# Kernel optimization log

Hardware: AMD Instinct MI355X
Metric: run time of the kernel (lower is better)

The kernel has to match this reference:

```python
import jax, jax.numpy as jnp
import numpy as np

T, HID = 2048, 1536
H, DK, DV = 12, 128, 128
KEY_DIM, VAL_DIM = H * DK, H * DV
CONV_K, GEN_RED = 4, 8
EPS = 1e-5


def setup_inputs() -> dict:
    key = jax.random.key(0)
    ks = jax.random.split(key, 12)
    def rn(k, sh, scale):
        return jax.random.normal(k, sh, dtype=jnp.float32) * scale
    inv = HID ** -0.5
    return {
        "hidden_states": rn(ks[0], (T, HID), 1.0),
        "Wq": rn(ks[1], (HID, KEY_DIM), inv),
        "Wk": rn(ks[2], (HID, KEY_DIM), inv),
        "Wv": rn(ks[3], (HID, VAL_DIM), inv),
        "Wb": rn(ks[4], (HID, H), inv),
        "Wa": rn(ks[5], (HID, H), inv),
        "A_log": jnp.log(jax.random.uniform(ks[6], (H,), minval=1e-3, maxval=16.0)),
        "dt_bias": jnp.ones((H,), jnp.float32),
        "Wg1": rn(ks[7], (HID, HID // GEN_RED), inv),
        "Wg2": rn(ks[8], (HID // GEN_RED, VAL_DIM * CONV_K), (HID // GEN_RED) ** -0.5),
        "Wgate": rn(ks[9], (HID, VAL_DIM), inv),
        "norm_weight": jnp.ones((DV,), jnp.float32),
        "Wo": rn(ks[10], (VAL_DIM, HID), VAL_DIM ** -0.5),
    }


def _dynamic_conv(v, hs, Wg1, Wg2):
    # per-token per-channel causal depthwise conv; kernels generated from hidden_states
    w = jax.nn.silu(hs @ Wg1) @ Wg2                    # (T, VAL_DIM*K)
    w = w.reshape(T, VAL_DIM, CONV_K)                  # (T, D, K)
    vpad = jnp.pad(v, ((CONV_K - 1, 0), (0, 0)))       # causal left pad
    windows = jnp.stack([vpad[i:i + T] for i in range(CONV_K)], axis=1)  # (T, K, D)
    return jax.nn.silu(jnp.einsum('tkd,tdk->td', windows, w))


def _gated_delta_rule(q, k, v, g, beta):
    # q,k: (T,H,DK); v: (T,H,DV); g,beta: (T,H)
    scale = DK ** -0.5
    def step(S, inp):
        q_t, k_t, v_t, g_t, b_t = inp
        S = S * jnp.exp(g_t)[:, None, None]            # decay state
        kv = jnp.einsum('hk,hkv->hv', k_t, S)          # k^T S
        S = S + jnp.einsum('hk,hv->hkv', k_t, (v_t - kv) * b_t[:, None])
        o_t = jnp.einsum('hk,hkv->hv', q_t, S) * scale
        return S, o_t
    S0 = jnp.zeros((H, DK, DV), jnp.float32)
    _, o = jax.lax.scan(step, S0, (q, k, v, g, beta))
    return o                                           # (T, H, DV)


def reference(hidden_states, Wq, Wk, Wv, Wb, Wa, A_log, dt_bias,
              Wg1, Wg2, Wgate, norm_weight, Wo):
    hs = hidden_states
    q = jax.nn.silu(hs @ Wq).reshape(T, H, DK)
    k = jax.nn.silu(hs @ Wk).reshape(T, H, DK)
    v = _dynamic_conv(hs @ Wv, hs, Wg1, Wg2).reshape(T, H, DV)
    beta = jax.nn.sigmoid(hs @ Wb)                           # (T, H)
    g = -jnp.exp(A_log) * jax.nn.softplus(hs @ Wa + dt_bias)  # (T, H) log-decay
    o = _gated_delta_rule(q, k, v, g, beta)                  # (T, H, DV)
    # gated RMSNorm over head_v_dim
    gate = (hs @ Wgate).reshape(T, H, DV)
    o = o * jax.lax.rsqrt(jnp.mean(o * o, axis=-1, keepdims=True) + EPS)
    o = o * norm_weight * (gate * jax.nn.sigmoid(gate))
    return o.reshape(T, VAL_DIM) @ Wo
```

## Files before the change

### kernel.cpp

```cpp
#include <hip/hip_runtime.h>
#include <hip/hip_bf16.h>
#include <math.h>

#define T     2048
#define HID   1536
#define NH    12
#define DK    128
#define DV    128
#define CONVK 4
#define CH    64
#define NC    32

typedef __attribute__((ext_vector_type(8))) short bf16x8;
typedef __attribute__((ext_vector_type(8))) _Float16 fp16x8;
typedef __attribute__((ext_vector_type(4))) float floatx4;

__device__ __forceinline__ float siluf(float x) {
    return x / (1.0f + __expf(-x));
}
__device__ __forceinline__ unsigned short f2bf(float f) {
    union { __hip_bfloat16 b; unsigned short u; } cv;
    cv.b = __float2bfloat16(f);
    return cv.u;
}
__device__ __forceinline__ float bf2f(unsigned short u) {
    union { unsigned int u; float f; } cv;
    cv.u = ((unsigned int)u) << 16;
    return cv.f;
}
__device__ __forceinline__ unsigned short f2h(float f) {
    union { _Float16 h; unsigned short u; } cv;
    cv.h = (_Float16)f;
    return cv.u;
}
__device__ __forceinline__ void gl_lds16(const void* g, void* l) {
    __builtin_amdgcn_global_load_lds(
        (const __attribute__((address_space(1))) void*)g,
        (__attribute__((address_space(3))) void*)l, 16, 0, 0);
}
__device__ __forceinline__ void split8_store(const float* xv,
                                             unsigned short* dh, unsigned short* dl) {
    ushort4 h0, h1, l0, l1;
    h0.x = f2bf(xv[0]); l0.x = f2bf(xv[0] - bf2f(h0.x));
    h0.y = f2bf(xv[1]); l0.y = f2bf(xv[1] - bf2f(h0.y));
    h0.z = f2bf(xv[2]); l0.z = f2bf(xv[2] - bf2f(h0.z));
    h0.w = f2bf(xv[3]); l0.w = f2bf(xv[3] - bf2f(h0.w));
    h1.x = f2bf(xv[4]); l1.x = f2bf(xv[4] - bf2f(h1.x));
    h1.y = f2bf(xv[5]); l1.y = f2bf(xv[5] - bf2f(h1.y));
    h1.z = f2bf(xv[6]); l1.z = f2bf(xv[6] - bf2f(h1.z));
    h1.w = f2bf(xv[7]); l1.w = f2bf(xv[7] - bf2f(h1.w));
    *(ushort4*)dh = h0; *(ushort4*)(dh + 4) = h1;
    *(ushort4*)dl = l0; *(ushort4*)(dl + 4) = l1;
}

__global__ __launch_bounds__(256) void splitcast3_kernel(const float* __restrict__ s,
                                                         unsigned short* __restrict__ hi,
                                                         unsigned short* __restrict__ lo,
                                                         unsigned short* __restrict__ h16,
                                                         int n4) {
    int i = blockIdx.x * 256 + threadIdx.x;
    if (i >= n4) return;
    float4 x = ((const float4*)s)[i];
    ushort4 h, l, f;
    h.x = f2bf(x.x); l.x = f2bf(x.x - bf2f(h.x)); f.x = f2h(x.x);
    h.y = f2bf(x.y); l.y = f2bf(x.y - bf2f(h.y)); f.y = f2h(x.y);
    h.z = f2bf(x.z); l.z = f2bf(x.z - bf2f(h.z)); f.z = f2h(x.z);
    h.w = f2bf(x.w); l.w = f2bf(x.w - bf2f(h.w)); f.w = f2h(x.w);
    ((ushort4*)hi)[i] = h;
    ((ushort4*)lo)[i] = l;
    ((ushort4*)h16)[i] = f;
}

__global__ __launch_bounds__(256) void transsplit_kernel(const float* __restrict__ src,
                                                         unsigned short* __restrict__ hi,
                                                         unsigned short* __restrict__ lo,
                                                         int K, int N) {
    __shared__ float tile[32][33];
    const int k0 = blockIdx.y * 32, n0 = blockIdx.x * 32;
    const int tx = threadIdx.x, ty = threadIdx.y;
#pragma unroll
    for (int r = 0; r < 4; ++r) {
        int kk = k0 + ty + 8 * r, nn = n0 + tx;
        tile[ty + 8 * r][tx] = (nn < N) ? src[(size_t)kk * N + nn] : 0.0f;
    }
    __syncthreads();
#pragma unroll
    for (int r = 0; r < 4; ++r) {
        int nn = n0 + ty + 8 * r, kk = k0 + tx;
        if (nn < N) {
            float x = tile[tx][ty + 8 * r];
            unsigned short h = f2bf(x);
            hi[(size_t)nn * K + kk] = h;
            lo[(size_t)nn * K + kk] = f2bf(x - bf2f(h));
        }
    }
}

__global__ __launch_bounds__(256) void transcasth_kernel(const float* __restrict__ src,
                                                         unsigned short* __restrict__ dst,
                                                         int K, int N) {
    __shared__ float tile[32][33];
    const int k0 = blockIdx.y * 32, n0 = blockIdx.x * 32;
    const int tx = threadIdx.x, ty = threadIdx.y;
#pragma unroll
    for (int r = 0; r < 4; ++r) {
        int kk = k0 + ty + 8 * r, nn = n0 + tx;
        tile[ty + 8 * r][tx] = (nn < N) ? src[(size_t)kk * N + nn] : 0.0f;
    }
    __syncthreads();
#pragma unroll
    for (int r = 0; r < 4; ++r) {
        int nn = n0 + ty + 8 * r, kk = k0 + tx;
        if (nn < N) dst[(size_t)nn * K + kk] = f2h(tile[tx][ty + 8 * r]);
    }
}

template<int EPI, int MODE>
__global__ __launch_bounds__(256)
void mgemm(const unsigned short* __restrict__ Ah, const unsigned short* __restrict__ Al,
           const unsigned short* __restrict__ Bh, const unsigned short* __restrict__ Bl,
           int K, int N, float* __restrict__ C, unsigned short* __restrict__ Cb,
           float* __restrict__ qf, float* __restrict__ vf, float* __restrict__ kf,
           unsigned short* __restrict__ gsilb, unsigned short* __restrict__ w1h16,
           float* __restrict__ bgraw)
{
    constexpr int BN   = MODE ? 64 : 128;
    constexpr int BCH  = BN / 16;
    constexpr int NFR  = MODE ? 2 : 4;
    __shared__ unsigned short AsH[2][4096];
    __shared__ unsigned short BsH[2][BCH * 512];
    __shared__ unsigned short AsL[MODE ? 2 : 1][MODE ? 4096 : 4];
    __shared__ unsigned short BsL[MODE ? 2 : 1][MODE ? BCH * 512 : 4];
    const int tid = threadIdx.x;
    const int wave = tid >> 6, lane = tid & 63;
    const int wr = wave >> 1, wc = wave & 1;
    const int lm = lane & 15, lq = lane >> 4;
    const int rowBase = blockIdx.y * 128, colBase = blockIdx.x * BN;

    floatx4 acc[4][NFR];
#pragma unroll
    for (int i = 0; i < 4; ++i)
#pragma unroll
        for (int j = 0; j < NFR; ++j) acc[i][j] = (floatx4){0.f, 0.f, 0.f, 0.f};

    const int mt0 = wave * 2, mt1 = wave * 2 + 1;
    const size_t aOff0 = (size_t)(rowBase + mt0 * 16 + lm) * K + lq * 8;
    const size_t aOff1 = (size_t)(rowBase + mt1 * 16 + lm) * K + lq * 8;
    const size_t bOff0 = (size_t)(colBase + mt0 * 16 + lm) * K + lq * 8;
    const size_t bOff1 = (size_t)(colBase + mt1 * 16 + lm) * K + lq * 8;
    const size_t bOffW = (size_t)(colBase + wave * 16 + lm) * K + lq * 8;

    auto STAGE = [&](int buf, int k0) {
        gl_lds16(Ah + aOff0 + k0, &AsH[buf][mt0 * 512]);
        gl_lds16(Ah + aOff1 + k0, &AsH[buf][mt1 * 512]);
        if (MODE) {
            gl_lds16(Al + aOff0 + k0, &AsL[buf][mt0 * 512]);
            gl_lds16(Al + aOff1 + k0, &AsL[buf][mt1 * 512]);
            gl_lds16(Bh + bOffW + k0, &BsH[buf][wave * 512]);
            gl_lds16(Bl + bOffW + k0, &BsL[buf][wave * 512]);
        } else {
            gl_lds16(Bh + bOff0 + k0, &BsH[buf][mt0 * 512]);
            gl_lds16(Bh + bOff1 + k0, &BsH[buf][mt1 * 512]);
        }
    };

    const int nIter = K >> 5;
    STAGE(0, 0);
    __syncthreads();
    int cur = 0;
    for (int it = 0; it < nIter; ++it) {
        if (it + 1 < nIter) STAGE(cur ^ 1, (it + 1) << 5);
        if (MODE == 0) {
            fp16x8 a[4], b[4];
#pragma unroll
            for (int i = 0; i < 4; ++i) {
                a[i] = *(const fp16x8*)&AsH[cur][(wr * 4 + i) * 512 + lane * 8];
                b[i] = *(const fp16x8*)&BsH[cur][(wc * 4 + i) * 512 + lane * 8];
            }
#pragma unroll
            for (int mi = 0; mi < 4; ++mi)
#pragma unroll
                for (int ni = 0; ni < 4; ++ni)
                    acc[mi][ni] = __builtin_amdgcn_mfma_f32_16x16x32_f16(
                        a[mi], b[ni], acc[mi][ni], 0, 0, 0);
        } else {
            bf16x8 ah[4], al[4], bh[2], bl[2];
#pragma unroll
            for (int i = 0; i < 4; ++i) {
                ah[i] = *(const bf16x8*)&AsH[cur][(wr * 4 + i) * 512 + lane * 8];
                al[i] = *(const bf16x8*)&AsL[cur][(wr * 4 + i) * 512 + lane * 8];
            }
#pragma unroll
            for (int j = 0; j < 2; ++j) {
                bh[j] = *(const bf16x8*)&BsH[cur][(wc * 2 + j) * 512 + lane * 8];
                bl[j] = *(const bf16x8*)&BsL[cur][(wc * 2 + j) * 512 + lane * 8];
            }
#pragma unroll
            for (int mi = 0; mi < 4; ++mi)
#pragma unroll
                for (int ni = 0; ni < 2; ++ni) {
                    acc[mi][ni] = __builtin_amdgcn_mfma_f32_16x16x32_bf16(
                        ah[mi], bh[ni], acc[mi][ni], 0, 0, 0);
                    acc[mi][ni] = __builtin_amdgcn_mfma_f32_16x16x32_bf16(
                        al[mi], bh[ni], acc[mi][ni], 0, 0, 0);
                    acc[mi][ni] = __builtin_amdgcn_mfma_f32_16x16x32_bf16(
                        ah[mi], bl[ni], acc[mi][ni], 0, 0, 0);
                }
        }
        __syncthreads();
        cur ^= 1;
    }

#pragma unroll
    for (int mi = 0; mi < 4; ++mi)
#pragma unroll
        for (int ni = 0; ni < NFR; ++ni) {
            const int col = colBase + wc * (NFR * 16) + ni * 16 + lm;
#pragma unroll
            for (int r = 0; r < 4; ++r) {
                const int row = rowBase + wr * 64 + mi * 16 + lq * 4 + r;
                const float x = acc[mi][ni][r];
                if (EPI == 0) {
                    C[(size_t)row * N + col] = x;
                } else if (EPI == 3) {
                    Cb[(size_t)row * N + col] = f2bf(x);
                } else if (EPI == 1) {
                    if (col < 1536)       qf[(size_t)row * 1536 + col] = siluf(x);
                    else if (col < 3072)  vf[(size_t)row * 1536 + col - 1536] = x;
                    else if (col < 4608)  gsilb[(size_t)row * 1536 + col - 3072] = f2bf(siluf(x));
                    else if (col < 4800)  w1h16[(size_t)row * 192 + col - 4608] = f2h(siluf(x));
                } else {
                    if (col < 1536)       kf[(size_t)row * 1536 + col] = siluf(x);
                    else if (col < 1560)  bgraw[(size_t)row * 24 + col - 1536] = x;
                }
            }
        }
}

__global__ __launch_bounds__(256) void bg2_kernel(const float* __restrict__ bgraw,
                                                  const float* __restrict__ A_log,
                                                  const float* __restrict__ dt_bias,
                                                  float* __restrict__ beta,
                                                  float* __restrict__ g) {
    int idx = blockIdx.x * 256 + threadIdx.x;
    if (idx >= T * 24) return;
    int t = idx / 24, c = idx % 24;
    float x = bgraw[idx];
    if (c < 12) {
        beta[t * NH + c] = 1.0f / (1.0f + __expf(-x));
    } else {
        int h = c - 12;
        float y = x + dt_bias[h];
        float sp = (y > 20.0f) ? y : log1pf(__expf(y));
        g[t * NH + h] = -__expf(A_log[h]) * sp;
    }
}

__global__ __launch_bounds__(256) void conv_kernel(const float* __restrict__ vpre,
                                                   const unsigned short* __restrict__ w,
                                                   float* __restrict__ v) {
    const int idx = blockIdx.x * 256 + threadIdx.x;
    if (idx >= T * HID) return;
    const int t = idx / HID, d = idx % HID;
    const ushort4 wv = *(const ushort4*)(w + (size_t)t * (HID * CONVK) + d * 4);
    const float w4[4] = { bf2f(wv.x), bf2f(wv.y), bf2f(wv.z), bf2f(wv.w) };
    float acc = 0.0f;
#pragma unroll
    for (int i = 0; i < CONVK; i++) {
        const int ts = t - (CONVK - 1) + i;
        if (ts >= 0) acc += vpre[(size_t)ts * HID + d] * w4[i];
    }
    v[idx] = siluf(acc);
}

__global__ __launch_bounds__(256) void prep_kernel(
    const float* __restrict__ q, const float* __restrict__ k,
    unsigned short* __restrict__ Qth, unsigned short* __restrict__ Qtl,
    unsigned short* __restrict__ Kth, unsigned short* __restrict__ Ktl)
{
    __shared__ float KT[128 * 68];
    const int c = blockIdx.x, h = blockIdx.y;
    const int tid = threadIdx.x;
    const size_t tb = (size_t)(h * NC + c) * 8192;

    {
        const int li = tid >> 2, lq4 = tid & 3;
        const float* src = k + (size_t)(c * CH + li) * HID + h * DK + lq4 * 32;
#pragma unroll
        for (int f = 0; f < 8; ++f) {
            float4 x = *(const float4*)(src + f * 4);
            int d0 = lq4 * 32 + f * 4;
            KT[(d0 + 0) * 68 + li] = x.x; KT[(d0 + 1) * 68 + li] = x.y;
            KT[(d0 + 2) * 68 + li] = x.z; KT[(d0 + 3) * 68 + li] = x.w;
        }
    }

#pragma unroll
    for (int e = 0; e < 4; ++e) {
        int u = e * 256 + tid;
        int ch = u >> 6, l = u & 63;
        int i = (ch >> 2) * 16 + (l & 15);
        int dbase = (ch & 3) * 32 + (l >> 4) * 8;
        const float* src = q + (size_t)(c * CH + i) * HID + h * DK + dbase;
        float4 a = *(const float4*)src, b = *(const float4*)(src + 4);
        float xv[8] = {a.x, a.y, a.z, a.w, b.x, b.y, b.z, b.w};
        split8_store(xv, &Qth[tb + ch * 512 + l * 8], &Qtl[tb + ch * 512 + l * 8]);
    }
    __syncthreads();

#pragma unroll
    for (int e = 0; e < 4; ++e) {
        int u = e * 256 + tid;
        int ch = u >> 6, l = u & 63;
        int dk = (ch >> 1) * 16 + (l & 15);
        int ibase = (ch & 1) * 32 + (l >> 4) * 8;
        float4 a = *(const float4*)&KT[dk * 68 + ibase];
        float4 b = *(const float4*)&KT[dk * 68 + ibase + 4];
        float xv[8] = {a.x, a.y, a.z, a.w, b.x, b.y, b.z, b.w};
        split8_store(xv, &Kth[tb + ch * 512 + l * 8], &Ktl[tb + ch * 512 + l * 8]);
    }
}

__global__ __launch_bounds__(256, 1) void chunkloc_kernel(
    const float* __restrict__ q, const float* __restrict__ k, const float* __restrict__ v,
    const float* __restrict__ g, const float* __restrict__ beta,
    float* __restrict__ X1g,
    unsigned short* __restrict__ X2th, unsigned short* __restrict__ X2tl,
    float* __restrict__ Mg, float* __restrict__ csg)
{
    __shared__ unsigned short KhS[64 * 136], KlS[64 * 136];
    __shared__ unsigned short QhS[64 * 136], QlS[64 * 136];
    __shared__ float KT[128 * 68];
    __shared__ float Vs[64 * 132];
    __shared__ float As[64 * 68];
    __shared__ float cs[64], sb[64], sbb[64];

    const int c = blockIdx.x, h = blockIdx.y;
    const int tid = threadIdx.x;
    const int wave = tid >> 6, lane = tid & 63;
    const int lm = lane & 15, lq = lane >> 4;
    const int li = tid >> 2, lq4 = tid & 3;
    const size_t rowbase = (size_t)(c * CH) * HID + h * DK;

    {
        const float* ksrc = k + rowbase + (size_t)li * HID + lq4 * 32;
        const float* qsrc = q + rowbase + (size_t)li * HID + lq4 * 32;
        const float* vsrc = v + (size_t)(c * CH + li) * HID + h * DV + lq4 * 32;
#pragma unroll
        for (int f = 0; f < 8; ++f) {
            float4 kx = *(const float4*)(ksrc + f * 4);
            float4 qx = *(const float4*)(qsrc + f * 4);
            float4 vx = *(const float4*)(vsrc + f * 4);
            const int d0 = lq4 * 32 + f * 4;
            {
                ushort4 hh, ll;
                hh.x = f2bf(kx.x); ll.x = f2bf(kx.x - bf2f(hh.x));
                hh.y = f2bf(kx.y); ll.y = f2bf(kx.y - bf2f(hh.y));
                hh.z = f2bf(kx.z); ll.z = f2bf(kx.z - bf2f(hh.z));
                hh.w = f2bf(kx.w); ll.w = f2bf(kx.w - bf2f(hh.w));
                *(ushort4*)&KhS[li * 136 + d0] = hh;
                *(ushort4*)&KlS[li * 136 + d0] = ll;
            }
            {
                ushort4 hh, ll;
                hh.x = f2bf(qx.x); ll.x = f2bf(qx.x - bf2f(hh.x));
                hh.y = f2bf(qx.y); ll.y = f2bf(qx.y - bf2f(hh.y));
                hh.z = f2bf(qx.z); ll.z = f2bf(qx.z - bf2f(hh.z));
                hh.w = f2bf(qx.w); ll.w = f2bf(qx.w - bf2f(hh.w));
                *(ushort4*)&QhS[li * 136 + d0] = hh;
                *(ushort4*)&QlS[li * 136 + d0] = ll;
            }
            KT[(d0 + 0) * 68 + li] = kx.x;
            KT[(d0 + 1) * 68 + li] = kx.y;
            KT[(d0 + 2) * 68 + li] = kx.z;
            KT[(d0 + 3) * 68 + li] = kx.w;
            *(float4*)&Vs[li * 132 + d0] = vx;
        }
    }
    if (tid < 64) {
        float gv = g[(c * CH + tid) * NH + h];
        float bv = beta[(c * CH + tid) * NH + h];
        float csv = gv;
#pragma unroll
        for (int off = 1; off < 64; off <<= 1) {
            float n = __shfl_up(csv, off);
            if (tid >= off) csv += n;
        }
        cs[tid] = csv; sb[tid] = bv; sbb[tid] = bv * __expf(csv);
    }
    __syncthreads();

    {
        const int ti = wave;
#pragma unroll
        for (int tj = 0; tj < 4; ++tj) {
            floatx4 acc = (floatx4){0.f, 0.f, 0.f, 0.f};
#pragma unroll
            for (int ks = 0; ks < 4; ++ks) {
                bf16x8 a_h = *(const bf16x8*)&KhS[(ti * 16 + lm) * 136 + ks * 32 + lq * 8];
                bf16x8 a_l = *(const bf16x8*)&KlS[(ti * 16 + lm) * 136 + ks * 32 + lq * 8];
                bf16x8 b_h = *(const bf16x8*)&KhS[(tj * 16 + lm) * 136 + ks * 32 + lq * 8];
                bf16x8 b_l = *(const bf16x8*)&KlS[(tj * 16 + lm) * 136 + ks * 32 + lq * 8];
                acc = __builtin_amdgcn_mfma_f32_16x16x32_bf16(a_h, b_h, acc, 0, 0, 0);
                acc = __builtin_amdgcn_mfma_f32_16x16x32_bf16(a_h, b_l, acc, 0, 0, 0);
                acc = __builtin_amdgcn_mfma_f32_16x16x32_bf16(a_l, b_h, acc, 0, 0, 0);
            }
#pragma unroll
            for (int r = 0; r < 4; ++r) {
                const int i = ti * 16 + lq * 4 + r, j = tj * 16 + lm;
                As[i * 68 + j] = (j < i) ? sb[i] * __expf(cs[i] - cs[j]) * acc[r] : 0.0f;
            }
        }
        const size_t mbase = (size_t)(h * NC + c) * CH * CH;
#pragma unroll
        for (int tj = 0; tj < 4; ++tj) {
            floatx4 acc = (floatx4){0.f, 0.f, 0.f, 0.f};
#pragma unroll
            for (int ks = 0; ks < 4; ++ks) {
                bf16x8 a_h = *(const bf16x8*)&QhS[(ti * 16 + lm) * 136 + ks * 32 + lq * 8];
                bf16x8 a_l = *(const bf16x8*)&QlS[(ti * 16 + lm) * 136 + ks * 32 + lq * 8];
                bf16x8 b_h = *(const bf16x8*)&KhS[(tj * 16 + lm) * 136 + ks * 32 + lq * 8];
                bf16x8 b_l = *(const bf16x8*)&KlS[(tj * 16 + lm) * 136 + ks * 32 + lq * 8];
                acc = __builtin_amdgcn_mfma_f32_16x16x32_bf16(a_h, b_h, acc, 0, 0, 0);
                acc = __builtin_amdgcn_mfma_f32_16x16x32_bf16(a_h, b_l, acc, 0, 0, 0);
                acc = __builtin_amdgcn_mfma_f32_16x16x32_bf16(a_l, b_h, acc, 0, 0, 0);
            }
#pragma unroll
            for (int r = 0; r < 4; ++r) {
                const int i = ti * 16 + lq * 4 + r, j = tj * 16 + lm;
                Mg[mbase + (size_t)i * 64 + j] =
                    (j <= i) ? __expf(cs[i] - cs[j]) * acc[r] : 0.0f;
            }
        }
    }

    float xc[64];
    const int col = tid;
    if (col < 128) {
#pragma unroll
        for (int i = 0; i < 64; ++i) xc[i] = sb[i] * Vs[i * 132 + col];
    } else {
        const int dcol = col - 128;
#pragma unroll
        for (int i4 = 0; i4 < 16; ++i4) {
            float4 kq = *(const float4*)&KT[dcol * 68 + i4 * 4];
            xc[i4 * 4 + 0] = sbb[i4 * 4 + 0] * kq.x;
            xc[i4 * 4 + 1] = sbb[i4 * 4 + 1] * kq.y;
            xc[i4 * 4 + 2] = sbb[i4 * 4 + 2] * kq.z;
            xc[i4 * 4 + 3] = sbb[i4 * 4 + 3] * kq.w;
        }
    }
    __syncthreads();

#pragma unroll
    for (int i = 1; i < 64; ++i) {
        float a = xc[i];
#pragma unroll
        for (int j4 = 0; j4 < (i + 3) / 4; ++j4) {
            float4 a4 = *(const float4*)&As[i * 68 + j4 * 4];
            a -= a4.x * xc[j4 * 4 + 0] + a4.y * xc[j4 * 4 + 1]
               + a4.z * xc[j4 * 4 + 2] + a4.w * xc[j4 * 4 + 3];
        }
        xc[i] = a;
    }

    {
        const size_t xbase = (size_t)(h * NC + c) * CH * 128;
        if (col < 128) {
            for (int i = 0; i < 64; ++i) X1g[xbase + (size_t)i * 128 + col] = xc[i];
        } else {
            for (int i = 0; i < 64; ++i) Vs[i * 132 + (col - 128)] = xc[i];
        }
    }
    if (tid < 64) csg[(size_t)(h * NC + c) * CH + tid] = cs[tid];
    __syncthreads();

    {
        const size_t tb = (size_t)(h * NC + c) * 8192;
#pragma unroll
        for (int e = 0; e < 4; ++e) {
            int u = e * 256 + tid;
            int ch = u >> 6, l = u & 63;
            int i = (ch >> 2) * 16 + (l & 15);
            int dbase = (ch & 3) * 32 + (l >> 4) * 8;
            float4 a = *(const float4*)&Vs[i * 132 + dbase];
            float4 b = *(const float4*)&Vs[i * 132 + dbase + 4];
            float xv[8] = {-a.x, -a.y, -a.z, -a.w, -b.x, -b.y, -b.z, -b.w};
            split8_store(xv, &X2th[tb + ch * 512 + l * 8], &X2tl[tb + ch * 512 + l * 8]);
        }
    }
}

__global__ __launch_bounds__(256, 1) void state_kernel(
    const unsigned short* __restrict__ Qth, const unsigned short* __restrict__ Qtl,
    const unsigned short* __restrict__ Kth, const unsigned short* __restrict__ Ktl,
    const unsigned short* __restrict__ X2th, const unsigned short* __restrict__ X2tl,
    float* __restrict__ X1g ,
    const float* __restrict__ csg, float* __restrict__ o)
{
    __shared__ unsigned short XAh[8192], XAl[8192];
    __shared__ unsigned short QAh[8192], QAl[8192];
    __shared__ unsigned short KAh[8192], KAl[8192];
    __shared__ unsigned short SBh[16 * 136], SBl[16 * 136];
    __shared__ unsigned short UBh[16 * 72],  UBl[16 * 72];
    __shared__ float St[16 * 132];
    __shared__ float scs[64];

    const int h = blockIdx.x, db = blockIdx.y;
    const int tid = threadIdx.x;
    const int wave = tid >> 6, lane = tid & 63;
    const int lm = lane & 15, lq = lane >> 4;

    for (int idx = tid; idx < 16 * 132; idx += 256) St[idx] = 0.0f;
    for (int idx = tid; idx < 16 * 136; idx += 256) { SBh[idx] = 0; SBl[idx] = 0; }
    __syncthreads();

    for (int c = 0; c < NC; ++c) {
        const size_t hc = (size_t)(h * NC + c);
        const size_t xb = hc * CH * 128;
        const size_t tb = hc * 8192 + (size_t)lane * 8;

        if (tid < 64) scs[tid] = csg[hc * CH + tid];
#pragma unroll
        for (int i2 = 0; i2 < 4; ++i2) {
            const int ch = wave * 4 + i2;
            gl_lds16(Qth  + tb + ch * 512, &QAh[ch * 512]);
            gl_lds16(Qtl  + tb + ch * 512, &QAl[ch * 512]);
            gl_lds16(X2th + tb + ch * 512, &XAh[ch * 512]);
            gl_lds16(X2tl + tb + ch * 512, &XAl[ch * 512]);
            gl_lds16(Kth  + tb + ch * 512, &KAh[ch * 512]);
            gl_lds16(Ktl  + tb + ch * 512, &KAl[ch * 512]);
        }
        __syncthreads();

        {
            const int mw = wave;
            float x1r[4];
#pragma unroll
            for (int r = 0; r < 4; ++r)
                x1r[r] = X1g[xb + (size_t)(mw * 16 + lq * 4 + r) * 128 + db * 16 + lm];
            floatx4 accU = (floatx4){0.f, 0.f, 0.f, 0.f};
            floatx4 accO = (floatx4){0.f, 0.f, 0.f, 0.f};
#pragma unroll
            for (int ks = 0; ks < 4; ++ks) {
                bf16x8 xh = *(const bf16x8*)&XAh[(mw * 4 + ks) * 512 + lane * 8];
                bf16x8 xl = *(const bf16x8*)&XAl[(mw * 4 + ks) * 512 + lane * 8];
                bf16x8 qh = *(const bf16x8*)&QAh[(mw * 4 + ks) * 512 + lane * 8];
                bf16x8 ql = *(const bf16x8*)&QAl[(mw * 4 + ks) * 512 + lane * 8];
                bf16x8 sh = *(const bf16x8*)&SBh[lm * 136 + ks * 32 + lq * 8];
                bf16x8 sl = *(const bf16x8*)&SBl[lm * 136 + ks * 32 + lq * 8];
                accU = __builtin_amdgcn_mfma_f32_16x16x32_bf16(xh, sh, accU, 0, 0, 0);
                accU = __builtin_amdgcn_mfma_f32_16x16x32_bf16(xh, sl, accU, 0, 0, 0);
                accU = __builtin_amdgcn_mfma_f32_16x16x32_bf16(xl, sh, accU, 0, 0, 0);
                accO = __builtin_amdgcn_mfma_f32_16x16x32_bf16(qh, sh, accO, 0, 0, 0);
                accO = __builtin_amdgcn_mfma_f32_16x16x32_bf16(qh, sl, accO, 0, 0, 0);
                accO = __builtin_amdgcn_mfma_f32_16x16x32_bf16(ql, sh, accO, 0, 0, 0);
            }
            const float cs63 = scs[63];
#pragma unroll
            for (int r = 0; r < 4; ++r) {
                const int row = mw * 16 + lq * 4 + r;
                const float u = accU[r] + x1r[r];
                X1g[xb + (size_t)row * 128 + db * 16 + lm] = u;
                const float up = u * __expf(cs63 - scs[row]);
                unsigned short uh = f2bf(up);
                UBh[lm * 72 + row] = uh;
                UBl[lm * 72 + row] = f2bf(up - bf2f(uh));
                o[(size_t)(c * CH + row) * HID + h * DV + db * 16 + lm] =
                    __expf(scs[row]) * accO[r];
            }
        }
        __syncthreads();

        {
            const float bC = __expf(scs[63]);
#pragma unroll
            for (int mt2 = 0; mt2 < 2; ++mt2) {
                const int mt = wave * 2 + mt2;
                floatx4 acc;
#pragma unroll
                for (int r = 0; r < 4; ++r)
                    acc[r] = bC * St[lm * 132 + mt * 16 + lq * 4 + r];
#pragma unroll
                for (int ks = 0; ks < 2; ++ks) {
                    bf16x8 ah = *(const bf16x8*)&KAh[(mt * 2 + ks) * 512 + lane * 8];
                    bf16x8 al = *(const bf16x8*)&KAl[(mt * 2 + ks) * 512 + lane * 8];
                    bf16x8 bh = *(const bf16x8*)&UBh[lm * 72 + ks * 32 + lq * 8];
                    bf16x8 bl = *(const bf16x8*)&UBl[lm * 72 + ks * 32 + lq * 8];
                    acc = __builtin_amdgcn_mfma_f32_16x16x32_bf16(ah, bh, acc, 0, 0, 0);
                    acc = __builtin_amdgcn_mfma_f32_16x16x32_bf16(ah, bl, acc, 0, 0, 0);
                    acc = __builtin_amdgcn_mfma_f32_16x16x32_bf16(al, bh, acc, 0, 0, 0);
                }
#pragma unroll
                for (int r = 0; r < 4; ++r) {
                    const int dk = mt * 16 + lq * 4 + r;
                    const float sv = acc[r];
                    St[lm * 132 + dk] = sv;
                    unsigned short sh = f2bf(sv);
                    SBh[lm * 136 + dk] = sh;
                    SBl[lm * 136 + dk] = f2bf(sv - bf2f(sh));
                }
            }
        }
        __syncthreads();
    }
}

__global__ __launch_bounds__(256) void outk_kernel(
    const float* __restrict__ Ug, const float* __restrict__ Mg,
    float* __restrict__ o)
{
    __shared__ float Msh[64 * 68];
    __shared__ float Ush[64 * 68];

    const int c = blockIdx.x, h = blockIdx.y;
    const int dvb = blockIdx.z * 64;
    const int tid = threadIdx.x;
    const size_t hc = (size_t)(h * NC + c);

    for (int e = 0; e < 16; ++e) {
        int idx = e * 256 + tid;
        Msh[(idx >> 6) * 68 + (idx & 63)] = Mg[hc * CH * CH + idx];
    }
    for (int e = 0; e < 16; ++e) {
        int idx = e * 256 + tid;
        int j = idx >> 6, cc = idx & 63;
        Ush[j * 68 + cc] = Ug[hc * CH * 128 + (size_t)j * 128 + dvb + cc];
    }
    __syncthreads();

    const int tx = tid & 15, ty = tid >> 4;
    const int c0 = tx * 4, i0 = ty * 4;
    float acc[4][4] = {{0}};
    for (int j4 = 0; j4 < 16; ++j4) {
        float uv[4][4];
#pragma unroll
        for (int s = 0; s < 4; ++s) {
            float4 u4 = *(const float4*)&Ush[(j4 * 4 + s) * 68 + c0];
            uv[s][0] = u4.x; uv[s][1] = u4.y; uv[s][2] = u4.z; uv[s][3] = u4.w;
        }
#pragma unroll
        for (int r = 0; r < 4; ++r) {
            float4 m4 = *(const float4*)&Msh[(i0 + r) * 68 + j4 * 4];
            const float mv[4] = {m4.x, m4.y, m4.z, m4.w};
#pragma unroll
            for (int s = 0; s < 4; ++s)
#pragma unroll
                for (int e = 0; e < 4; ++e) acc[r][e] += mv[s] * uv[s][e];
        }
    }
    const float scale = 0.08838834764831845f;
#pragma unroll
    for (int r = 0; r < 4; ++r) {
        float* op = &o[(size_t)(c * CH + i0 + r) * HID + h * DV + dvb + c0];
        float4 prev = *(const float4*)op;
        float4 ov = make_float4(scale * (prev.x + acc[r][0]),
                                scale * (prev.y + acc[r][1]),
                                scale * (prev.z + acc[r][2]),
                                scale * (prev.w + acc[r][3]));
        *(float4*)op = ov;
    }
}

__global__ __launch_bounds__(256) void normgate_kernel(const float* __restrict__ o,
                                                       const unsigned short* __restrict__ gsil,
                                                       const float* __restrict__ nw,
                                                       unsigned short* __restrict__ out_hi,
                                                       unsigned short* __restrict__ out_lo) {
    const int gw = (blockIdx.x * 256 + threadIdx.x) >> 6;
    const int lane = threadIdx.x & 63;
    if (gw >= T * NH) return;
    const int t = gw / NH, h = gw % NH;
    const size_t base = (size_t)t * HID + h * DV;
    const float a = o[base + lane];
    const float b = o[base + lane + 64];
    float ss = a * a + b * b;
    ss += __shfl_xor(ss, 1);  ss += __shfl_xor(ss, 2);  ss += __shfl_xor(ss, 4);
    ss += __shfl_xor(ss, 8);  ss += __shfl_xor(ss, 16); ss += __shfl_xor(ss, 32);
    const float r = rsqrtf(ss * (1.0f / 128.0f) + 1e-5f);
    float va = a * r * nw[lane]      * bf2f(gsil[base + lane]);
    float vb = b * r * nw[lane + 64] * bf2f(gsil[base + lane + 64]);
    unsigned short ha = f2bf(va), hb = f2bf(vb);
    out_hi[base + lane]      = ha;  out_lo[base + lane]      = f2bf(va - bf2f(ha));
    out_hi[base + lane + 64] = hb;  out_lo[base + lane + 64] = f2bf(vb - bf2f(hb));
}

extern "C" void kernel_launch(void* const* d_in, const int* in_sizes, int n_in,
                              void* d_out, int out_size, void* d_ws, size_t ws_size,
                              hipStream_t stream) {
    const float* hs      = (const float*)d_in[0];
    const float* Wq      = (const float*)d_in[1];
    const float* Wk      = (const float*)d_in[2];
    const float* Wv      = (const float*)d_in[3];
    const float* Wb      = (const float*)d_in[4];
    const float* Wa      = (const float*)d_in[5];
    const float* A_log   = (const float*)d_in[6];
    const float* dt_bias = (const float*)d_in[7];
    const float* Wg1     = (const float*)d_in[8];
    const float* Wg2     = (const float*)d_in[9];
    const float* Wgate   = (const float*)d_in[10];
    const float* norm_w  = (const float*)d_in[11];
    const float* Wo      = (const float*)d_in[12];

    float* ws = (float*)d_ws;
    float* q    = ws;
    float* kbuf = ws + 3145728;
    float* vpre = ws + 6291456;
    float* vbuf = ws + 9437184;
    unsigned short* gsil = (unsigned short*)(ws + 12582912);
    float* X1g  = ws + 14155776;
    unsigned short* X2th = (unsigned short*)(ws + 17301504);
    unsigned short* X2tl = (unsigned short*)(ws + 18874368);
    float* Mg   = ws + 20447232;
    unsigned short* WTAfh = (unsigned short*)(ws + 14155776);
    unsigned short* WTBh  = (unsigned short*)(ws + 17891328);
    unsigned short* WTBl  = (unsigned short*)(ws + 19169280);
    unsigned short* wcv   = (unsigned short*)(ws + 14155776);
    unsigned short* WG2h  = (unsigned short*)(ws + 22044672);
    unsigned short* hsh   = (unsigned short*)(ws + 22634496);
    unsigned short* w1h16 = (unsigned short*)(ws + 24207360);
    float* bgraw = ws + 24403968;
    unsigned short* Kth = (unsigned short*)(ws + 22044672);
    unsigned short* Ktl = (unsigned short*)(ws + 23617536);
    float* beta  = ws + 25190400;
    float* g     = ws + 25214976;
    float* csg   = ws + 25239552;
    unsigned short* hsbh = (unsigned short*)(ws + 9437184);
    unsigned short* hsbl = (unsigned short*)(ws + 11010048);
    unsigned short* Qth  = (unsigned short*)(ws + 6291456);
    unsigned short* Qtl  = (unsigned short*)(ws + 7864320);
    unsigned short* WoTh = (unsigned short*)(ws);
    unsigned short* WoTl = (unsigned short*)(ws + 1179648);
    unsigned short* onh  = (unsigned short*)(ws + 6291456);
    unsigned short* onl  = (unsigned short*)(ws + 7864320);

    const dim3 blk(256);
    const dim3 blkT(32, 8);

    splitcast3_kernel<<<3072, blk, 0, stream>>>(hs, hsbh, hsbl, hsh, (T * HID) / 4);
    transcasth_kernel<<<dim3(48, 48), blkT, 0, stream>>>(Wq,    WTAfh,               1536, 1536);
    transcasth_kernel<<<dim3(48, 48), blkT, 0, stream>>>(Wv,    WTAfh + 1536 * 1536, 1536, 1536);
    transcasth_kernel<<<dim3(48, 48), blkT, 0, stream>>>(Wgate, WTAfh + 3072 * 1536, 1536, 1536);
    transcasth_kernel<<<dim3(6, 48),  blkT, 0, stream>>>(Wg1,   WTAfh + 4608 * 1536, 1536, 192);
    transsplit_kernel<<<dim3(48, 48), blkT, 0, stream>>>(Wk, WTBh,               WTBl,               1536, 1536);
    transsplit_kernel<<<dim3(1, 48),  blkT, 0, stream>>>(Wb, WTBh + 1536 * 1536, WTBl + 1536 * 1536, 1536, 12);
    transsplit_kernel<<<dim3(1, 48),  blkT, 0, stream>>>(Wa, WTBh + 1548 * 1536, WTBl + 1548 * 1536, 1536, 12);
    transcasth_kernel<<<dim3(192, 6), blkT, 0, stream>>>(Wg2, WG2h, 192, 6144);

    mgemm<1, 0><<<dim3(38, 16), blk, 0, stream>>>(hsh, nullptr, WTAfh, nullptr, 1536, 4864,
        nullptr, nullptr, q, vpre, nullptr, gsil, w1h16, nullptr);
    mgemm<2, 1><<<dim3(26, 16), blk, 0, stream>>>(hsbh, hsbl, WTBh, WTBl, 1536, 1664,
        nullptr, nullptr, nullptr, nullptr, kbuf, nullptr, nullptr, bgraw);
    bg2_kernel<<<192, blk, 0, stream>>>(bgraw, A_log, dt_bias, beta, g);

    mgemm<3, 0><<<dim3(48, 16), blk, 0, stream>>>(w1h16, nullptr, WG2h, nullptr, 192, 6144,
        nullptr, wcv, nullptr, nullptr, nullptr, nullptr, nullptr, nullptr);
    conv_kernel<<<(T * HID) / 256, blk, 0, stream>>>(vpre, wcv, vbuf);

    chunkloc_kernel<<<dim3(NC, NH), blk, 0, stream>>>(q, kbuf, vbuf, g, beta,
                                                      X1g, X2th, X2tl, Mg, csg);
    prep_kernel<<<dim3(NC, NH), blk, 0, stream>>>(q, kbuf, Qth, Qtl, Kth, Ktl);
    state_kernel<<<dim3(NH, 8), blk, 0, stream>>>(Qth, Qtl, Kth, Ktl, X2th, X2tl,
                                                  X1g, csg, vbuf);
    transsplit_kernel<<<dim3(48, 48), blkT, 0, stream>>>(Wo, WoTh, WoTl, 1536, 1536);
    outk_kernel<<<dim3(NC, NH, 2), blk, 0, stream>>>(X1g, Mg, vbuf);

    normgate_kernel<<<6144, blk, 0, stream>>>(vbuf, gsil, norm_w, onh, onl);
    mgemm<0, 1><<<dim3(24, 16), blk, 0, stream>>>(onh, onl, WoTh, WoTl, 1536, 1536,
        (float*)d_out, nullptr, nullptr, nullptr, nullptr, nullptr, nullptr, nullptr);
}
```

Measured before the change: 566.5 us.

## Load state-kernel operands directly into registers and keep state in accumulators

The sequential chunk-state kernel stops staging Q/K/X2 hi/lo tiles through LDS and has each wave load its MFMA operand fragments straight from global memory into registers. The fp32 state tile moves from shared memory into per-wave accumulator registers, and the bf16 split state is written with vectorized ushort4 stores. This drops one barrier per chunk and the LDS round trip on a latency-bound serial loop. In exchange, register pressure rises and each chunk's global loads are no longer issued asynchronously ahead of the barrier.

```diff
diff --git a/kernel.cpp b/kernel.cpp
--- a/kernel.cpp
+++ b/kernel.cpp
@@ -498,108 +498,105 @@
     float* __restrict__ X1g ,
     const float* __restrict__ csg, float* __restrict__ o)
 {
-    __shared__ unsigned short XAh[8192], XAl[8192];
-    __shared__ unsigned short QAh[8192], QAl[8192];
-    __shared__ unsigned short KAh[8192], KAl[8192];
     __shared__ unsigned short SBh[16 * 136], SBl[16 * 136];
     __shared__ unsigned short UBh[16 * 72],  UBl[16 * 72];
-    __shared__ float St[16 * 132];
-    __shared__ float scs[64];
 
     const int h = blockIdx.x, db = blockIdx.y;
     const int tid = threadIdx.x;
     const int wave = tid >> 6, lane = tid & 63;
     const int lm = lane & 15, lq = lane >> 4;
 
-    for (int idx = tid; idx < 16 * 132; idx += 256) St[idx] = 0.0f;
     for (int idx = tid; idx < 16 * 136; idx += 256) { SBh[idx] = 0; SBl[idx] = 0; }
+    floatx4 st0 = (floatx4){0.f, 0.f, 0.f, 0.f};
+    floatx4 st1 = (floatx4){0.f, 0.f, 0.f, 0.f};
     __syncthreads();
 
     for (int c = 0; c < NC; ++c) {
         const size_t hc = (size_t)(h * NC + c);
         const size_t xb = hc * CH * 128;
         const size_t tb = hc * 8192 + (size_t)lane * 8;
-
-        if (tid < 64) scs[tid] = csg[hc * CH + tid];
-#pragma unroll
-        for (int i2 = 0; i2 < 4; ++i2) {
-            const int ch = wave * 4 + i2;
-            gl_lds16(Qth  + tb + ch * 512, &QAh[ch * 512]);
-            gl_lds16(Qtl  + tb + ch * 512, &QAl[ch * 512]);
-            gl_lds16(X2th + tb + ch * 512, &XAh[ch * 512]);
-            gl_lds16(X2tl + tb + ch * 512, &XAl[ch * 512]);
-            gl_lds16(Kth  + tb + ch * 512, &KAh[ch * 512]);
-            gl_lds16(Ktl  + tb + ch * 512, &KAl[ch * 512]);
-        }
-        __syncthreads();
+        const int mw = wave;
+
+        bf16x8 xa_h[4], xa_l[4], qa_h[4], qa_l[4], ka_h[4], ka_l[4];
+#pragma unroll
+        for (int ks = 0; ks < 4; ++ks) {
+            const size_t off = tb + (size_t)(mw * 4 + ks) * 512;
+            xa_h[ks] = *(const bf16x8*)(X2th + off);
+            xa_l[ks] = *(const bf16x8*)(X2tl + off);
+            qa_h[ks] = *(const bf16x8*)(Qth + off);
+            qa_l[ks] = *(const bf16x8*)(Qtl + off);
+            ka_h[ks] = *(const bf16x8*)(Kth + off);
+            ka_l[ks] = *(const bf16x8*)(Ktl + off);
+        }
+        float x1r[4], csr[4];
+#pragma unroll
+        for (int r = 0; r < 4; ++r) {
+            const int row = mw * 16 + lq * 4 + r;
+            x1r[r] = X1g[xb + (size_t)row * 128 + db * 16 + lm];
+            csr[r] = csg[hc * CH + row];
+        }
+        const float cs63 = csg[hc * CH + 63];
 
         {
-            const int mw = wave;
-            float x1r[4];
-#pragma unroll
-            for (int r = 0; r < 4; ++r)
-                x1r[r] = X1g[xb + (size_t)(mw * 16 + lq * 4 + r) * 128 + db * 16 + lm];
             floatx4 accU = (floatx4){0.f, 0.f, 0.f, 0.f};
             floatx4 accO = (floatx4){0.f, 0.f, 0.f, 0.f};
 #pragma unroll
             for (int ks = 0; ks < 4; ++ks) {
-                bf16x8 xh = *(const bf16x8*)&XAh[(mw * 4 + ks) * 512 + lane * 8];
-                bf16x8 xl = *(const bf16x8*)&XAl[(mw * 4 + ks) * 512 + lane * 8];
-                bf16x8 qh = *(const bf16x8*)&QAh[(mw * 4 + ks) * 512 + lane * 8];
-                bf16x8 ql = *(const bf16x8*)&QAl[(mw * 4 + ks) * 512 + lane * 8];
                 bf16x8 sh = *(const bf16x8*)&SBh[lm * 136 + ks * 32 + lq * 8];
                 bf16x8 sl = *(const bf16x8*)&SBl[lm * 136 + ks * 32 + lq * 8];
-                accU = __builtin_amdgcn_mfma_f32_16x16x32_bf16(xh, sh, accU, 0, 0, 0);
-                accU = __builtin_amdgcn_mfma_f32_16x16x32_bf16(xh, sl, accU, 0, 0, 0);
-                accU = __builtin_amdgcn_mfma_f32_16x16x32_bf16(xl, sh, accU, 0, 0, 0);
-                accO = __builtin_amdgcn_mfma_f32_16x16x32_bf16(qh, sh, accO, 0, 0, 0);
-                accO = __builtin_amdgcn_mfma_f32_16x16x32_bf16(qh, sl, accO, 0, 0, 0);
-                accO = __builtin_amdgcn_mfma_f32_16x16x32_bf16(ql, sh, accO, 0, 0, 0);
-            }
-            const float cs63 = scs[63];
+                accU = __builtin_amdgcn_mfma_f32_16x16x32_bf16(xa_h[ks], sh, accU, 0, 0, 0);
+                accU = __builtin_amdgcn_mfma_f32_16x16x32_bf16(xa_h[ks], sl, accU, 0, 0, 0);
+                accU = __builtin_amdgcn_mfma_f32_16x16x32_bf16(xa_l[ks], sh, accU, 0, 0, 0);
+                accO = __builtin_amdgcn_mfma_f32_16x16x32_bf16(qa_h[ks], sh, accO, 0, 0, 0);
+                accO = __builtin_amdgcn_mfma_f32_16x16x32_bf16(qa_h[ks], sl, accO, 0, 0, 0);
+                accO = __builtin_amdgcn_mfma_f32_16x16x32_bf16(qa_l[ks], sh, accO, 0, 0, 0);
+            }
 #pragma unroll
             for (int r = 0; r < 4; ++r) {
                 const int row = mw * 16 + lq * 4 + r;
                 const float u = accU[r] + x1r[r];
                 X1g[xb + (size_t)row * 128 + db * 16 + lm] = u;
-                const float up = u * __expf(cs63 - scs[row]);
+                const float up = u * __expf(cs63 - csr[r]);
                 unsigned short uh = f2bf(up);
                 UBh[lm * 72 + row] = uh;
                 UBl[lm * 72 + row] = f2bf(up - bf2f(uh));
                 o[(size_t)(c * CH + row) * HID + h * DV + db * 16 + lm] =
-                    __expf(scs[row]) * accO[r];
+                    __expf(csr[r]) * accO[r];
             }
         }
         __syncthreads();
 
         {
-            const float bC = __expf(scs[63]);
+            const float bC = __expf(cs63);
 #pragma unroll
             for (int mt2 = 0; mt2 < 2; ++mt2) {
                 const int mt = wave * 2 + mt2;
                 floatx4 acc;
-#pragma unroll
-                for (int r = 0; r < 4; ++r)
-                    acc[r] = bC * St[lm * 132 + mt * 16 + lq * 4 + r];
+                floatx4 stc = mt2 ? st1 : st0;
+#pragma unroll
+                for (int r = 0; r < 4; ++r) acc[r] = bC * stc[r];
 #pragma unroll
                 for (int ks = 0; ks < 2; ++ks) {
-                    bf16x8 ah = *(const bf16x8*)&KAh[(mt * 2 + ks) * 512 + lane * 8];
-                    bf16x8 al = *(const bf16x8*)&KAl[(mt * 2 + ks) * 512 + lane * 8];
+                    bf16x8 ah = ka_h[mt2 * 2 + ks];
+                    bf16x8 al = ka_l[mt2 * 2 + ks];
                     bf16x8 bh = *(const bf16x8*)&UBh[lm * 72 + ks * 32 + lq * 8];
                     bf16x8 bl = *(const bf16x8*)&UBl[lm * 72 + ks * 32 + lq * 8];
                     acc = __builtin_amdgcn_mfma_f32_16x16x32_bf16(ah, bh, acc, 0, 0, 0);
                     acc = __builtin_amdgcn_mfma_f32_16x16x32_bf16(ah, bl, acc, 0, 0, 0);
                     acc = __builtin_amdgcn_mfma_f32_16x16x32_bf16(al, bh, acc, 0, 0, 0);
                 }
+                if (mt2) st1 = acc; else st0 = acc;
+                ushort4 shv, slv;
 #pragma unroll
                 for (int r = 0; r < 4; ++r) {
-                    const int dk = mt * 16 + lq * 4 + r;
                     const float sv = acc[r];
-                    St[lm * 132 + dk] = sv;
                     unsigned short sh = f2bf(sv);
-                    SBh[lm * 136 + dk] = sh;
-                    SBl[lm * 136 + dk] = f2bf(sv - bf2f(sh));
+                    ((unsigned short*)&shv)[r] = sh;
+                    ((unsigned short*)&slv)[r] = f2bf(sv - bf2f(sh));
                 }
+                const int dkb = mt * 16 + lq * 4;
+                *(ushort4*)&SBh[lm * 136 + dkb] = shv;
+                *(ushort4*)&SBl[lm * 136 + dkb] = slv;
             }
         }
         __syncthreads();
```

Result: slower. 585.5 us (+3.4%).
